# Kernel tuning notes

Measured on AMD Instinct MI355X. Metric: run time of the kernel, lower is better.

The kernel has to match this reference:

```python
import jax, jax.numpy as jnp
import numpy as np

TOPK = 4  # constructor default topk=4


def setup_inputs() -> dict:
    key = jax.random.key(0)
    k_x, k_a, k_b, k_w, k_bias = jax.random.split(key, 5)
    b, s, h, j, a, r = 4, 2048, 2048, 2048, 64, 16
    x = jax.random.normal(k_x, (b, s, h), dtype=jnp.float32)
    A = jax.random.normal(k_a, (a, r, h), dtype=jnp.float32) * 0.02   # adapter down-proj bank
    B = jax.random.normal(k_b, (a, j, r), dtype=jnp.float32) * 0.02   # adapter up-proj bank
    W = jax.random.normal(k_w, (j, h), dtype=jnp.float32) * 0.02      # base Linear weight
    bias = jax.random.normal(k_bias, (j,), dtype=jnp.float32) * 0.02  # base Linear bias
    return {"x": x, "A": A, "B": B, "W": W, "bias": bias}


def reference(x, A, B, W, bias):
    # vecs: per-adapter low-rank projections of each token. [b,s,a,r]
    vecs = jnp.einsum('arh,bsh->bsar', A, x)
    # routing score = L2 norm over rank dim. [b,s,a]
    arrows = jnp.linalg.norm(vecs, axis=-1)
    # top-k adapters per token -> uniform 1/topk routing weights (scatter of a constant,
    # so no gradient flows through the routing weights, matching torch semantics).
    _, idx = jax.lax.top_k(arrows, TOPK)                     # [b,s,topk]
    routes = jax.nn.one_hot(idx, arrows.shape[-1], dtype=x.dtype).sum(-2) / TOPK  # [b,s,a]
    # weighted combine of selected adapter vecs. [b,s,r]
    v = jnp.einsum('bsa,bsar->bsr', routes, vecs)
    # delta = (routes-weighted B) applied to v; contract over a then r without
    # materializing the [b,s,j,r] intermediate. [b,s,j]
    delta = jnp.einsum('bsa,ajr,bsr->bsj', routes, B, v)
    base = jnp.einsum('bsh,jh->bsj', x, W) + bias
    return base + delta
```

## Files before the change

### kernel.cpp

```cpp
#include <hip/hip_runtime.h>
#include <hip/hip_bf16.h>
#include <stdint.h>

#define TOKENS 8192
#define H 2048
#define JDIM 2048
#define NADAPT 64
#define RANK 16
#define KG 1024
#define KTOT 3072
#define NT2 48
#define NT1 64

typedef __bf16 v8bf __attribute__((ext_vector_type(8)));
typedef float v4f __attribute__((ext_vector_type(4)));
typedef unsigned short us8 __attribute__((ext_vector_type(8)));
typedef unsigned short us4 __attribute__((ext_vector_type(4)));

__device__ __forceinline__ unsigned short f2bf(float f) {
  union { __bf16 b; unsigned short u; } c; c.b = (__bf16)f; return c.u;
}
__device__ __forceinline__ float bf2f(unsigned short u) {
  union { unsigned int u; float f; } c; c.u = ((unsigned int)u) << 16; return c.f;
}

__device__ __forceinline__ us8 pack8(float4 a, float4 b) {
  us8 r;
  r[0]=f2bf(a.x); r[1]=f2bf(a.y); r[2]=f2bf(a.z); r[3]=f2bf(a.w);
  r[4]=f2bf(b.x); r[5]=f2bf(b.y); r[6]=f2bf(b.z); r[7]=f2bf(b.w);
  return r;
}

__device__ __forceinline__ void split8(float4 a, float4 b, us8& h, us8& l) {
  float v[8] = {a.x, a.y, a.z, a.w, b.x, b.y, b.z, b.w};
  #pragma unroll
  for (int i = 0; i < 8; ++i) {
    h[i] = f2bf(v[i]);
    l[i] = f2bf(v[i] - bf2f(h[i]));
  }
}

__global__ void cast_all_kernel(const float* __restrict__ x,
                                const float* __restrict__ A,
                                const float* __restrict__ W,
                                const float* __restrict__ Bsrc,
                                unsigned short* __restrict__ XG,
                                unsigned short* __restrict__ XLO,
                                unsigned short* __restrict__ Ahi,
                                unsigned short* __restrict__ Alo,
                                unsigned short* __restrict__ WB) {
  int bid = blockIdx.x;
  int cg = threadIdx.x;
  if (bid < TOKENS) {
    int row = bid;
    const float4* s = (const float4*)(x + ((size_t)row << 11) + ((size_t)cg << 3));
    float4 a = s[0], b = s[1];
    us8 h, l;
    split8(a, b, h, l);
    *(us8*)(XG  + (size_t)row * KTOT + ((size_t)cg << 3)) = h;
    *(us8*)(XLO + (size_t)row * H    + ((size_t)cg << 3)) = l;
  } else if (bid < TOKENS + KG) {
    int row = bid - TOKENS;
    const float4* s = (const float4*)(A + ((size_t)row << 11) + ((size_t)cg << 3));
    float4 a = s[0], b = s[1];
    us8 h, l;
    split8(a, b, h, l);
    *(us8*)(Ahi + ((size_t)row << 11) + ((size_t)cg << 3)) = h;
    *(us8*)(Alo + ((size_t)row << 11) + ((size_t)cg << 3)) = l;
  } else if (bid < TOKENS + KG + JDIM) {
    int row = bid - TOKENS - KG;
    const float4* s = (const float4*)(W + ((size_t)row << 11) + ((size_t)cg << 3));
    float4 a = s[0], b = s[1];
    *(us8*)(WB + (size_t)row * KTOT + ((size_t)cg << 3)) = pack8(a, b);
  } else {
    int idx = (bid - TOKENS - KG - JDIM) * 256 + cg;
    int a = idx >> 11, j = idx & 2047;
    const float4* s = (const float4*)(Bsrc + (((size_t)a << 11) + j) * RANK);
    float4 f0 = s[0], f1 = s[1], f2 = s[2], f3 = s[3];
    us8* d = (us8*)(WB + (size_t)j * KTOT + H + a * RANK);
    d[0] = pack8(f0, f1);
    d[1] = pack8(f2, f3);
  }
}

__global__ void route_kernel(const float* __restrict__ vecs,
                             unsigned short* __restrict__ XG) {
  __shared__ float vsh[4][16];
  int wave = threadIdx.x >> 6, lane = threadIdx.x & 63;
  int t = blockIdx.x * 4 + wave;
  const float* vrow = vecs + (size_t)t * KG;
  const float4* vp = (const float4*)(vrow + lane * RANK);
  float4 q0 = vp[0], q1 = vp[1], q2 = vp[2], q3 = vp[3];
  float ss = q0.x*q0.x + q0.y*q0.y + q0.z*q0.z + q0.w*q0.w
           + q1.x*q1.x + q1.y*q1.y + q1.z*q1.z + q1.w*q1.w
           + q2.x*q2.x + q2.y*q2.y + q2.z*q2.z + q2.w*q2.w
           + q3.x*q3.x + q3.y*q3.y + q3.z*q3.z + q3.w*q3.w;
  float arr = ss;
  int sel[4];
  #pragma unroll
  for (int k = 0; k < 4; ++k) {
    float m = arr; int mi = lane;
    #pragma unroll
    for (int o = 32; o > 0; o >>= 1) {
      float om = __shfl_xor(m, o);
      int oi  = __shfl_xor(mi, o);
      if (om > m || (om == m && oi < mi)) { m = om; mi = oi; }
    }
    sel[k] = mi;
    if (lane == mi) arr = -3.0e38f;
  }
  if (lane < 16) {
    float s = vrow[sel[0]*RANK + lane] + vrow[sel[1]*RANK + lane]
            + vrow[sel[2]*RANK + lane] + vrow[sel[3]*RANK + lane];
    vsh[wave][lane] = 0.0625f * s;
  }
  __syncthreads();
  bool on = (lane == sel[0]) | (lane == sel[1]) | (lane == sel[2]) | (lane == sel[3]);
  us8 lo, hi;
  #pragma unroll
  for (int r = 0; r < 8; ++r) lo[r] = on ? f2bf(vsh[wave][r])     : (unsigned short)0;
  #pragma unroll
  for (int r = 0; r < 8; ++r) hi[r] = on ? f2bf(vsh[wave][r + 8]) : (unsigned short)0;
  us8* d = (us8*)(XG + (size_t)t * KTOT + H + lane * RANK);
  d[0] = lo; d[1] = hi;
}

__device__ __forceinline__ void gload_lds16(const void* gsrc, void* ldst) {
  __builtin_amdgcn_global_load_lds(
      (const __attribute__((address_space(1))) unsigned int*)gsrc,
      (__attribute__((address_space(3))) unsigned int*)ldst, 16, 0, 0);
}

#define BAR()  asm volatile("s_waitcnt vmcnt(0) lgkmcnt(0)\n\ts_barrier" ::: "memory")
#define BARO() asm volatile("s_barrier" ::: "memory")
#define VM4() asm volatile("s_waitcnt vmcnt(4)" ::: "memory")
#define P1() __builtin_amdgcn_s_setprio(1)
#define P0() __builtin_amdgcn_s_setprio(0)

#define MM1(mi, xf, bv) do {                                                   \
  acc[mi][0] = __builtin_amdgcn_mfma_f32_16x16x32_bf16(xf, bv[0], acc[mi][0], 0, 0, 0); \
  acc[mi][1] = __builtin_amdgcn_mfma_f32_16x16x32_bf16(xf, bv[1], acc[mi][1], 0, 0, 0); \
  acc[mi][2] = __builtin_amdgcn_mfma_f32_16x16x32_bf16(xf, bv[2], acc[mi][2], 0, 0, 0); \
  acc[mi][3] = __builtin_amdgcn_mfma_f32_16x16x32_bf16(xf, bv[3], acc[mi][3], 0, 0, 0); \
} while (0)

#define S_XH1(B, kel) gload_lds16(XhB + (size_t)srow * KTOT + (kel) + scol, (B) + tid*16)
#define S_XH2(B, kel) gload_lds16(XhB + (size_t)(srow + 128) * KTOT + (kel) + scol, (B) + 8192 + tid*16)
#define S_XL1(B, kel) gload_lds16(XlB + (size_t)srow * H + (kel) + scol, (B) + 16384 + tid*16)
#define S_XL2(B, kel) gload_lds16(XlB + (size_t)(srow + 128) * H + (kel) + scol, (B) + 24576 + tid*16)
#define S_AH1(B, kel) gload_lds16(AhB + (size_t)srow * H + (kel) + scol, (B) + 32768 + tid*16)
#define S_AL1(B, kel) gload_lds16(AlB + (size_t)srow * H + (kel) + scol, (B) + 40960 + tid*16)

#define TILE1(AHC, AHN, kel) do {                                              \
                    \
  P1(); MM1(0, xh[0], AHC); MM1(1, xh[1], AHC);                                \
        MM1(2, xh[2], AHC); MM1(3, xh[3], AHC); P0();                          \
  _Pragma("unroll")                                                            \
  for (int j = 0; j < 4; ++j) al[j] = *(const v8bf*)(bufA + 40960 + bbyte + j * 1024); \
  S_XH1(bufC, kel); S_XH2(bufC, kel);                                          \
                             \
  P1(); MM1(0, xh[0], al); MM1(1, xh[1], al);                                  \
        MM1(2, xh[2], al); MM1(3, xh[3], al); P0();                            \
  _Pragma("unroll")                                                            \
  for (int i = 0; i < 4; ++i) xl[i] = *(const v8bf*)(bufA + 16384 + abyte + i * 1024); \
  S_AH1(bufC, kel); S_XL1(bufC, kel);                                          \
  VM4(); BARO();                                                               \
                 \
  P1(); MM1(0, xl[0], AHC); MM1(1, xl[1], AHC);                                \
        MM1(2, xl[2], AHC); MM1(3, xl[3], AHC); P0();                          \
  _Pragma("unroll")                                                            \
  for (int i = 0; i < 4; ++i) xh[i] = *(const v8bf*)(bufB + abyte + i * 1024); \
  _Pragma("unroll")                                                            \
  for (int j = 0; j < 4; ++j) AHN[j] = *(const v8bf*)(bufB + 32768 + bbyte + j * 1024); \
  S_XL2(bufC, kel); S_AL1(bufC, kel);                                          \
  VM4(); BARO();                                                               \
  { char* tmp_ = bufA; bufA = bufB; bufB = bufC; bufC = tmp_; }                \
} while (0)

__global__ __launch_bounds__(512, 1) void gemm1_8ph_kernel(
    const unsigned short* __restrict__ Xhi,
    const unsigned short* __restrict__ Xlo,
    const unsigned short* __restrict__ Ahi,
    const unsigned short* __restrict__ Alo,
    float* __restrict__ C) {
  __shared__ char Ls[147456];
  const int tid = threadIdx.x;
  const int lane = tid & 63, wid = tid >> 6;
  const int wr = wid >> 1, wc = wid & 1;
  const int rA = lane & 15, grp = lane >> 4;
  const int grpx = (grp ^ ((rA >> 1) & 3)) << 4;

  const int bid = blockIdx.x;
  const int g = bid & 7, r = bid >> 3;
  const int bm = g * 4 + (r & 3), bn = r >> 2;

  const unsigned short* XhB = Xhi + (size_t)(bm * 256) * KTOT;
  const unsigned short* XlB = Xlo + (size_t)(bm * 256) * H;
  const unsigned short* AhB = Ahi + (size_t)(bn * 128) * H;
  const unsigned short* AlB = Alo + (size_t)(bn * 128) * H;

  const int srow = tid >> 2;
  const int scol = ((tid & 3) ^ ((tid >> 3) & 3)) << 3;

  const int abyte = (wr * 64 + rA) * 64 + grpx;
  const int bbyte = (wc * 64 + rA) * 64 + grpx;

  char* bufA = Ls;
  char* bufB = Ls + 49152;
  char* bufC = Ls + 98304;

  v4f acc[4][4];
  #pragma unroll
  for (int i = 0; i < 4; ++i)
    #pragma unroll
    for (int j = 0; j < 4; ++j)
      acc[i][j] = (v4f){0.f, 0.f, 0.f, 0.f};
  v8bf xh[4], xl[4], al[4], ahA[4], ahB_[4];

  S_XH1(bufA, 0); S_XH2(bufA, 0); S_AH1(bufA, 0); S_XL1(bufA, 0); S_XL2(bufA, 0); S_AL1(bufA, 0);
  S_XH1(bufB, 32); S_XH2(bufB, 32); S_AH1(bufB, 32); S_XL1(bufB, 32); S_XL2(bufB, 32); S_AL1(bufB, 32);
  BAR();
  #pragma unroll
  for (int i = 0; i < 4; ++i) xh[i] = *(const v8bf*)(bufA + abyte + i * 1024);
  #pragma unroll
  for (int j = 0; j < 4; ++j) ahA[j] = *(const v8bf*)(bufA + 32768 + bbyte + j * 1024);

  #pragma unroll 1
  for (int t = 0; t < NT1; t += 2) {
    const int ka = (t + 2 < NT1 ? t + 2 : NT1 - 1) * 32;
    const int kb = (t + 3 < NT1 ? t + 3 : NT1 - 1) * 32;
    TILE1(ahA, ahB_, ka);
    TILE1(ahB_, ahA, kb);
  }

  const int row0 = bm * 256 + wr * 64 + (grp << 2);
  const int col0 = bn * 128 + wc * 64 + rA;
  #pragma unroll
  for (int mi = 0; mi < 4; ++mi)
    #pragma unroll
    for (int j = 0; j < 4; ++j)
      #pragma unroll
      for (int q = 0; q < 4; ++q)
        C[(size_t)(row0 + mi * 16 + q) * KG + col0 + j * 16] = acc[mi][j][q];
}

#define STAGE(regionUS, panel, kelem) do {                                        \
  gload_lds16((panel) + aoff0 + (kelem), (char*)(regionUS) + tid * 16);           \
  gload_lds16((panel) + aoff1 + (kelem), (char*)(regionUS) + 8192 + tid * 16);    \
} while (0)

#define PHO(AFC, BFC, RA, AFN, RB, BFN, STG) do {                                 \
  P1();                                                                           \
  _Pragma("unroll")                                                               \
  for (int i = 0; i < 4; ++i)                                                     \
    _Pragma("unroll")                                                             \
    for (int j = 0; j < 4; ++j)                                                   \
      acc[i][j] = __builtin_amdgcn_mfma_f32_16x16x32_bf16(                        \
          AFC[i], BFC[j], acc[i][j], 0, 0, 0);                                    \
  P0();                                                                           \
  _Pragma("unroll")                                                               \
  for (int i = 0; i < 4; ++i)                                                     \
    AFN[i] = *(const v8bf*)((const char*)(RA) + abyte + (4 + i) * 1024);          \
  _Pragma("unroll")                                                               \
  for (int j = 0; j < 4; ++j)                                                     \
    BFN[j] = *(const v8bf*)((const char*)(RB) + bbyte + j * 1024);                \
  STG;                                                                            \
} while (0)

#define PHE(AFC, BFC, RA, AFN, STG) do {                                          \
  P1();                                                                           \
  _Pragma("unroll")                                                               \
  for (int i = 0; i < 4; ++i)                                                     \
    _Pragma("unroll")                                                             \
    for (int j = 0; j < 4; ++j)                                                   \
      acc[4 + i][j] = __builtin_amdgcn_mfma_f32_16x16x32_bf16(                    \
          AFC[i], BFC[j], acc[4 + i][j], 0, 0, 0);                                \
  P0();                                                                           \
  _Pragma("unroll")                                                               \
  for (int i = 0; i < 4; ++i)                                                     \
    AFN[i] = *(const v8bf*)((const char*)(RA) + abyte + i * 1024);                \
  STG;                                                                            \
  VM4(); BARO();                                                                  \
} while (0)

__global__ __launch_bounds__(512, 1) void gemm2_8ph_kernel(
    const unsigned short* __restrict__ Xg, const unsigned short* __restrict__ Wb,
    float* __restrict__ C, const float* __restrict__ bias) {
  __shared__ unsigned short lds[65536];
  const int tid = threadIdx.x;
  const int lane = tid & 63, wid = tid >> 6;
  const int wr = wid >> 2, wc = wid & 3;
  const int rA = lane & 15, grp = lane >> 4;
  const int grpx = (grp ^ ((rA >> 1) & 3)) << 4;

  const int bid = blockIdx.x;
  const int g = bid & 7, r = bid >> 3;
  const int bm = g * 4 + (r & 3), bn = r >> 2;

  const unsigned short* Ap = Xg + (size_t)(bm * 256) * KTOT;
  const unsigned short* Bp = Wb + (size_t)(bn * 256) * KTOT;

  const int srow = tid >> 2;
  const int scol = ((tid & 3) ^ ((tid >> 3) & 3)) << 3;
  const size_t aoff0 = (size_t)srow * KTOT + scol;
  const size_t aoff1 = (size_t)(srow + 128) * KTOT + scol;

  unsigned short* A0k0 = lds;
  unsigned short* A0k1 = lds + 8192;
  unsigned short* B0k0 = lds + 16384;
  unsigned short* B0k1 = lds + 24576;
  unsigned short* A1k0 = lds + 32768;
  unsigned short* A1k1 = lds + 40960;
  unsigned short* B1k0 = lds + 49152;
  unsigned short* B1k1 = lds + 57344;

  const int abyte = (wr * 128 + rA) * 64 + grpx;
  const int bbyte = (wc * 64 + rA) * 64 + grpx;

  v4f acc[8][4];
  #pragma unroll
  for (int i = 0; i < 8; ++i)
    #pragma unroll
    for (int j = 0; j < 4; ++j)
      acc[i][j] = (v4f){0.f, 0.f, 0.f, 0.f};
  v8bf afA[4], afB[4], bfrA[4], bfrB[4];

  STAGE(A0k0, Ap, 0);
  STAGE(B0k0, Bp, 0);
  STAGE(A0k1, Ap, 32);
  STAGE(B0k1, Bp, 32);
  STAGE(A1k0, Ap, 64);
  STAGE(B1k0, Bp, 64);
  BAR();
  #pragma unroll
  for (int i = 0; i < 4; ++i) afA[i] = *(const v8bf*)((const char*)A0k0 + abyte + i * 1024);
  #pragma unroll
  for (int j = 0; j < 4; ++j) bfrA[j] = *(const v8bf*)((const char*)B0k0 + bbyte + j * 1024);

  #pragma unroll 1
  for (int t = 0; t < NT2; t += 2) {
    const int k1a = (t + 1) * 64 + 32;
    const int k0a = (t + 2 < NT2 ? t + 2 : NT2 - 1) * 64;
    const int k1b = (t + 2 < NT2 ? t + 2 : NT2 - 1) * 64 + 32;
    const int k0b = (t + 3 < NT2 ? t + 3 : NT2 - 1) * 64;
    PHO(afA, bfrA, A0k0, afB, B0k1, bfrB, STAGE(A1k1, Ap, k1a));
    PHE(afB, bfrA, A0k1, afA, STAGE(B1k1, Bp, k1a));
    PHO(afA, bfrB, A0k1, afB, B1k0, bfrA, STAGE(A0k0, Ap, k0a));
    PHE(afB, bfrB, A1k0, afA, STAGE(B0k0, Bp, k0a));
    PHO(afA, bfrA, A1k0, afB, B1k1, bfrB, STAGE(A0k1, Ap, k1b));
    PHE(afB, bfrA, A1k1, afA, STAGE(B0k1, Bp, k1b));
    PHO(afA, bfrB, A1k1, afB, B0k0, bfrA, STAGE(A1k0, Ap, k0b));
    PHE(afB, bfrB, A0k0, afA, STAGE(B1k0, Bp, k0b));
  }

  const int row0 = bm * 256 + wr * 128 + (grp << 2);
  const int col0 = bn * 256 + wc * 64 + rA;
  float bv[4];
  #pragma unroll
  for (int j = 0; j < 4; ++j) bv[j] = bias[col0 + j * 16];
  #pragma unroll
  for (int mi = 0; mi < 8; ++mi)
    #pragma unroll
    for (int j = 0; j < 4; ++j)
      #pragma unroll
      for (int q = 0; q < 4; ++q)
        C[(size_t)(row0 + mi * 16 + q) * JDIM + col0 + j * 16] = acc[mi][j][q] + bv[j];
}

extern "C" void kernel_launch(void* const* d_in, const int* in_sizes, int n_in,
                              void* d_out, int out_size, void* d_ws, size_t ws_size,
                              hipStream_t stream) {
  const float* x    = (const float*)d_in[0];
  const float* A    = (const float*)d_in[1];
  const float* Bb   = (const float*)d_in[2];
  const float* W    = (const float*)d_in[3];
  const float* bias = (const float*)d_in[4];
  float* out = (float*)d_out;

  char* ws = (char*)d_ws;
  unsigned short* XG  = (unsigned short*)ws;
  unsigned short* WB  = (unsigned short*)(ws + (size_t)48 * 1024 * 1024);
  unsigned short* Ahi = (unsigned short*)(ws + (size_t)60 * 1024 * 1024);
  unsigned short* Alo = (unsigned short*)(ws + (size_t)64 * 1024 * 1024);
  float* vecs         = (float*)d_out;
  unsigned short* XLO = (unsigned short*)((char*)d_out + (size_t)32 * 1024 * 1024);

  cast_all_kernel<<<TOKENS + KG + JDIM + 512, 256, 0, stream>>>(
      x, A, W, Bb, XG, XLO, Ahi, Alo, WB);

  gemm1_8ph_kernel<<<256, 512, 0, stream>>>(XG, XLO, Ahi, Alo, vecs);

  route_kernel<<<TOKENS / 4, 256, 0, stream>>>(vecs, XG);

  gemm2_8ph_kernel<<<256, 512, 0, stream>>>(XG, WB, out, bias);
}
```

Baseline: 212.0 us.

## Switch gemm2 main loop to 32x32x16 bf16 MFMA tiles

Rewrites the second GEMM's inner loop to use 32x32x16 bf16 MFMA instructions instead of 16x16x32. Each wave now holds a 4x2 grid of 16-float accumulators, and fragment reads, swizzled LDS offsets, phase macros and the epilogue store mapping are reorganized to match. The phase structure changes so that a barrier follows every phase, with a vmcnt(6) wait. Larger MFMA tiles need fewer LDS fragment reads per FLOP and fewer instructions, but the extra barriers and changed register pressure could add stalls.

New measurement: 224.6 us. 1.06x slower.

```diff
diff --git a/kernel.cpp b/kernel.cpp
--- a/kernel.cpp
+++ b/kernel.cpp
@@ -14,6 +14,7 @@
 
 typedef __bf16 v8bf __attribute__((ext_vector_type(8)));
 typedef float v4f __attribute__((ext_vector_type(4)));
+typedef float v16f __attribute__((ext_vector_type(16)));
 typedef unsigned short us8 __attribute__((ext_vector_type(8)));
 typedef unsigned short us4 __attribute__((ext_vector_type(4)));
 
@@ -134,6 +135,7 @@
 #define BAR()  asm volatile("s_waitcnt vmcnt(0) lgkmcnt(0)\n\ts_barrier" ::: "memory")
 #define BARO() asm volatile("s_barrier" ::: "memory")
 #define VM4() asm volatile("s_waitcnt vmcnt(4)" ::: "memory")
+#define VM6() asm volatile("s_waitcnt vmcnt(6)" ::: "memory")
 #define P1() __builtin_amdgcn_s_setprio(1)
 #define P0() __builtin_amdgcn_s_setprio(0)
 
@@ -152,20 +154,17 @@
 #define S_AL1(B, kel) gload_lds16(AlB + (size_t)srow * H + (kel) + scol, (B) + 40960 + tid*16)
 
 #define TILE1(AHC, AHN, kel) do {                                              \
-                    \
   P1(); MM1(0, xh[0], AHC); MM1(1, xh[1], AHC);                                \
         MM1(2, xh[2], AHC); MM1(3, xh[3], AHC); P0();                          \
   _Pragma("unroll")                                                            \
   for (int j = 0; j < 4; ++j) al[j] = *(const v8bf*)(bufA + 40960 + bbyte + j * 1024); \
   S_XH1(bufC, kel); S_XH2(bufC, kel);                                          \
-                             \
   P1(); MM1(0, xh[0], al); MM1(1, xh[1], al);                                  \
         MM1(2, xh[2], al); MM1(3, xh[3], al); P0();                            \
   _Pragma("unroll")                                                            \
   for (int i = 0; i < 4; ++i) xl[i] = *(const v8bf*)(bufA + 16384 + abyte + i * 1024); \
   S_AH1(bufC, kel); S_XL1(bufC, kel);                                          \
   VM4(); BARO();                                                               \
-                 \
   P1(); MM1(0, xl[0], AHC); MM1(1, xl[1], AHC);                                \
         MM1(2, xl[2], AHC); MM1(3, xl[3], AHC); P0();                          \
   _Pragma("unroll")                                                            \
@@ -249,38 +248,46 @@
   gload_lds16((panel) + aoff1 + (kelem), (char*)(regionUS) + 8192 + tid * 16);    \
 } while (0)
 
-#define PHO(AFC, BFC, RA, AFN, RB, BFN, STG) do {                                 \
+#define MM32(mi, nj, af_, bf_) \
+  acc[mi][nj] = __builtin_amdgcn_mfma_f32_32x32x16_bf16(af_, bf_, acc[mi][nj], 0, 0, 0)
+
+#define AFRD(dst, R, mibase) do {                                                 \
+  dst[0] = *(const v8bf*)((const char*)(R) + abase + (mibase)*2048 + psl0);       \
+  dst[1] = *(const v8bf*)((const char*)(R) + abase + (mibase)*2048 + psl1);       \
+  dst[2] = *(const v8bf*)((const char*)(R) + abase + (mibase+1)*2048 + psl0);     \
+  dst[3] = *(const v8bf*)((const char*)(R) + abase + (mibase+1)*2048 + psl1);     \
+} while (0)
+
+#define BFRD(R) do {                                                              \
+  bfr[0] = *(const v8bf*)((const char*)(R) + bbase + psl0);                       \
+  bfr[1] = *(const v8bf*)((const char*)(R) + bbase + psl1);                       \
+  bfr[2] = *(const v8bf*)((const char*)(R) + bbase + 2048 + psl0);                \
+  bfr[3] = *(const v8bf*)((const char*)(R) + bbase + 2048 + psl1);                \
+} while (0)
+
+#define PH2A(RAn, STG) do {                                                       \
   P1();                                                                           \
-  _Pragma("unroll")                                                               \
-  for (int i = 0; i < 4; ++i)                                                     \
-    _Pragma("unroll")                                                             \
-    for (int j = 0; j < 4; ++j)                                                   \
-      acc[i][j] = __builtin_amdgcn_mfma_f32_16x16x32_bf16(                        \
-          AFC[i], BFC[j], acc[i][j], 0, 0, 0);                                    \
+  MM32(0, 0, afA[0], bfr[0]); MM32(0, 1, afA[0], bfr[2]);                         \
+  MM32(1, 0, afA[2], bfr[0]); MM32(1, 1, afA[2], bfr[2]);                         \
+  MM32(0, 0, afA[1], bfr[1]); MM32(0, 1, afA[1], bfr[3]);                         \
+  MM32(1, 0, afA[3], bfr[1]); MM32(1, 1, afA[3], bfr[3]);                         \
   P0();                                                                           \
-  _Pragma("unroll")                                                               \
-  for (int i = 0; i < 4; ++i)                                                     \
-    AFN[i] = *(const v8bf*)((const char*)(RA) + abyte + (4 + i) * 1024);          \
-  _Pragma("unroll")                                                               \
-  for (int j = 0; j < 4; ++j)                                                     \
-    BFN[j] = *(const v8bf*)((const char*)(RB) + bbyte + j * 1024);                \
+  AFRD(afB, RAn, 2);                                                              \
   STG;                                                                            \
-} while (0)
-
-#define PHE(AFC, BFC, RA, AFN, STG) do {                                          \
+  VM6(); BARO();                                                                  \
+} while (0)
+
+#define PH2B(RBn, RAn, STG) do {                                                  \
   P1();                                                                           \
-  _Pragma("unroll")                                                               \
-  for (int i = 0; i < 4; ++i)                                                     \
-    _Pragma("unroll")                                                             \
-    for (int j = 0; j < 4; ++j)                                                   \
-      acc[4 + i][j] = __builtin_amdgcn_mfma_f32_16x16x32_bf16(                    \
-          AFC[i], BFC[j], acc[4 + i][j], 0, 0, 0);                                \
+  MM32(2, 0, afB[0], bfr[0]); MM32(2, 1, afB[0], bfr[2]);                         \
+  MM32(3, 0, afB[2], bfr[0]); MM32(3, 1, afB[2], bfr[2]);                         \
+  MM32(2, 0, afB[1], bfr[1]); MM32(2, 1, afB[1], bfr[3]);                         \
+  MM32(3, 0, afB[3], bfr[1]); MM32(3, 1, afB[3], bfr[3]);                         \
   P0();                                                                           \
-  _Pragma("unroll")                                                               \
-  for (int i = 0; i < 4; ++i)                                                     \
-    AFN[i] = *(const v8bf*)((const char*)(RA) + abyte + i * 1024);                \
+  BFRD(RBn);                                                                      \
+  AFRD(afA, RAn, 0);                                                              \
   STG;                                                                            \
-  VM4(); BARO();                                                                  \
+  VM6(); BARO();                                                                  \
 } while (0)
 
 __global__ __launch_bounds__(512, 1) void gemm2_8ph_kernel(
@@ -290,8 +297,13 @@
   const int tid = threadIdx.x;
   const int lane = tid & 63, wid = tid >> 6;
   const int wr = wid >> 2, wc = wid & 3;
-  const int rA = lane & 15, grp = lane >> 4;
-  const int grpx = (grp ^ ((rA >> 1) & 3)) << 4;
+
+  const int l31 = lane & 31, hi5 = lane >> 5;
+  const int xr = (l31 >> 1) & 3;
+  const int psl0 = ((0 + hi5) ^ xr) << 4;
+  const int psl1 = ((2 + hi5) ^ xr) << 4;
+  const int abase = (wr * 128 + l31) * 64;
+  const int bbase = (wc * 64 + l31) * 64;
 
   const int bid = blockIdx.x;
   const int g = bid & 7, r = bid >> 3;
@@ -314,16 +326,15 @@
   unsigned short* B1k0 = lds + 49152;
   unsigned short* B1k1 = lds + 57344;
 
-  const int abyte = (wr * 128 + rA) * 64 + grpx;
-  const int bbyte = (wc * 64 + rA) * 64 + grpx;
-
-  v4f acc[8][4];
-  #pragma unroll
-  for (int i = 0; i < 8; ++i)
+  v16f acc[4][2];
+  #pragma unroll
+  for (int i = 0; i < 4; ++i)
     #pragma unroll
-    for (int j = 0; j < 4; ++j)
-      acc[i][j] = (v4f){0.f, 0.f, 0.f, 0.f};
-  v8bf afA[4], afB[4], bfrA[4], bfrB[4];
+    for (int j = 0; j < 2; ++j)
+      #pragma unroll
+      for (int q = 0; q < 16; ++q)
+        acc[i][j][q] = 0.f;
+  v8bf afA[4], afB[4], bfr[4];
 
   STAGE(A0k0, Ap, 0);
   STAGE(B0k0, Bp, 0);
@@ -332,10 +343,8 @@
   STAGE(A1k0, Ap, 64);
   STAGE(B1k0, Bp, 64);
   BAR();
-  #pragma unroll
-  for (int i = 0; i < 4; ++i) afA[i] = *(const v8bf*)((const char*)A0k0 + abyte + i * 1024);
-  #pragma unroll
-  for (int j = 0; j < 4; ++j) bfrA[j] = *(const v8bf*)((const char*)B0k0 + bbyte + j * 1024);
+  AFRD(afA, A0k0, 0);
+  BFRD(B0k0);
 
   #pragma unroll 1
   for (int t = 0; t < NT2; t += 2) {
@@ -343,28 +352,31 @@
     const int k0a = (t + 2 < NT2 ? t + 2 : NT2 - 1) * 64;
     const int k1b = (t + 2 < NT2 ? t + 2 : NT2 - 1) * 64 + 32;
     const int k0b = (t + 3 < NT2 ? t + 3 : NT2 - 1) * 64;
-    PHO(afA, bfrA, A0k0, afB, B0k1, bfrB, STAGE(A1k1, Ap, k1a));
-    PHE(afB, bfrA, A0k1, afA, STAGE(B1k1, Bp, k1a));
-    PHO(afA, bfrB, A0k1, afB, B1k0, bfrA, STAGE(A0k0, Ap, k0a));
-    PHE(afB, bfrB, A1k0, afA, STAGE(B0k0, Bp, k0a));
-    PHO(afA, bfrA, A1k0, afB, B1k1, bfrB, STAGE(A0k1, Ap, k1b));
-    PHE(afB, bfrA, A1k1, afA, STAGE(B0k1, Bp, k1b));
-    PHO(afA, bfrB, A1k1, afB, B0k0, bfrA, STAGE(A1k0, Ap, k0b));
-    PHE(afB, bfrB, A0k0, afA, STAGE(B1k0, Bp, k0b));
-  }
-
-  const int row0 = bm * 256 + wr * 128 + (grp << 2);
-  const int col0 = bn * 256 + wc * 64 + rA;
-  float bv[4];
-  #pragma unroll
-  for (int j = 0; j < 4; ++j) bv[j] = bias[col0 + j * 16];
-  #pragma unroll
-  for (int mi = 0; mi < 8; ++mi)
+    PH2A(A0k0, STAGE(A1k1, Ap, k1a));
+    PH2B(B0k1, A0k1, STAGE(B1k1, Bp, k1a));
+    PH2A(A0k1, STAGE(A0k0, Ap, k0a));
+    PH2B(B1k0, A1k0, STAGE(B0k0, Bp, k0a));
+    PH2A(A1k0, STAGE(A0k1, Ap, k1b));
+    PH2B(B1k1, A1k1, STAGE(B0k1, Bp, k1b));
+    PH2A(A1k1, STAGE(A1k0, Ap, k0b));
+    PH2B(B0k0, A0k0, STAGE(B1k0, Bp, k0b));
+  }
+
+  const int row0 = bm * 256 + wr * 128 + (hi5 << 2);
+  const int col0 = bn * 256 + wc * 64 + l31;
+  float bv0 = bias[col0];
+  float bv1 = bias[col0 + 32];
+  #pragma unroll
+  for (int mi = 0; mi < 4; ++mi)
     #pragma unroll
-    for (int j = 0; j < 4; ++j)
+    for (int nj = 0; nj < 2; ++nj) {
+      float bv = nj ? bv1 : bv0;
       #pragma unroll
-      for (int q = 0; q < 4; ++q)
-        C[(size_t)(row0 + mi * 16 + q) * JDIM + col0 + j * 16] = acc[mi][j][q] + bv[j];
+      for (int reg = 0; reg < 16; ++reg) {
+        int rr = row0 + mi * 32 + (reg & 3) + ((reg >> 2) << 3);
+        C[(size_t)rr * JDIM + col0 + nj * 32] = acc[mi][nj][reg] + bv;
+      }
+    }
 }
 
 extern "C" void kernel_launch(void* const* d_in, const int* in_sizes, int n_in,
```
